# Kernel optimization log

Measured on AMD Instinct MI355X. Metric: run time of the kernel, lower is better.

The kernel has to match this reference:

```python
import jax, jax.numpy as jnp
import numpy as np

B, N, F_IN = 8, 4096, 128
H0, H1, OUT = 64, 32, 32
DENSITY = 0.004  # avg degree ~16


def setup_inputs() -> dict:
    key = jax.random.key(0)
    ks = jax.random.split(key, 8)
    x = jax.random.normal(ks[0], (B, N, F_IN), dtype=jnp.float32)
    # sparse binary adjacency (graph structure), stored dense as the module does
    adj = (jax.random.uniform(ks[1], (B, N, N)) < DENSITY).astype(jnp.float32)
    def w(k, i, o):
        return jax.random.normal(k, (i, o), dtype=jnp.float32) * (1.0 / np.sqrt(i))
    return {
        "x": x, "adj": adj,
        "Ws0": w(ks[2], F_IN, H0), "Wn0": w(ks[3], F_IN, H0), "b0": jnp.zeros((H0,), jnp.float32),
        "Ws1": w(ks[4], H0, H1),   "Wn1": w(ks[5], H0, H1),   "b1": jnp.zeros((H1,), jnp.float32),
        "Ws2": w(ks[6], H1, OUT),  "Wn2": w(ks[7], H1, OUT),  "b2": jnp.zeros((OUT,), jnp.float32),
    }


def _sage_layer(h, adj, deg_inv, Ws, Wn, b):
    # mean over incoming neighbors: row j of adj selects messages into node j
    neigh = jnp.einsum('bij,bjd->bid', adj, h) * deg_inv  # [B,N,d_in]
    return jax.nn.relu(h @ Ws + neigh @ Wn + b)


def reference(x, adj, Ws0, Wn0, b0, Ws1, Wn1, b1, Ws2, Wn2, b2):
    deg = jnp.sum(adj, axis=-1, keepdims=True)  # [B,N,1] in-degree
    deg_inv = 1.0 / jnp.maximum(deg, 1.0)
    h = _sage_layer(x, adj, deg_inv, Ws0, Wn0, b0)
    h = _sage_layer(h, adj, deg_inv, Ws1, Wn1, b1)
    h = _sage_layer(h, adj, deg_inv, Ws2, Wn2, b2)
    # original flattens to [B*N, out_dim] embeddings
    return h.reshape(B * N, -1)
```

## Files before the change

### kernel.cpp

```cpp
#include <hip/hip_runtime.h>
#include <hip/hip_bf16.h>

#define BN      32768
#define NCOL    4096
#define MAX_NBR 64

#define WS_NBR 0
#define WS_DEG (4*1024*1024)
#define WS_H0  (WS_DEG + 131072)
#define WS_H1  (WS_H0 + 8*1024*1024)

__global__ __launch_bounds__(256) void build_csr_kernel(
    const float* __restrict__ adj,
    unsigned short* __restrict__ nbr,
    int* __restrict__ deg)
{
    const int wave = threadIdx.x >> 6, lane = threadIdx.x & 63;
    const int row  = (blockIdx.x << 2) + wave;
    const float4* arow = reinterpret_cast<const float4*>(adj + (size_t)row * NCOL);
    unsigned short* outrow = nbr + (size_t)row * MAX_NBR;
    const unsigned long long below = (1ull << lane) - 1ull;

    int cnt = 0;
    #pragma unroll 4
    for (int t = 0; t < 16; ++t) {
        const int c = t * 64 + lane;
        const float4 q = arow[c];
        const float v[4] = { q.x, q.y, q.z, q.w };
        #pragma unroll
        for (int e = 0; e < 4; ++e) {
            const bool nz = (v[e] != 0.0f);
            const unsigned long long m = __ballot(nz);
            if (nz) {
                const int pos = cnt + (int)__popcll(m & below);
                if (pos < MAX_NBR) outrow[pos] = (unsigned short)(c * 4 + e);
            }
            cnt += (int)__popcll(m);
        }
    }
    if (lane == 0) deg[row] = cnt;
}

template<int D_IN, int D_OUT>
__global__ __launch_bounds__(256) void gather_layer_kernel(
    const float* __restrict__ hin,
    const unsigned short* __restrict__ nbr,
    const int* __restrict__ deg,
    const float* __restrict__ Ws, const float* __restrict__ Wn,
    const float* __restrict__ bias,
    float* __restrict__ hout)
{
    __shared__ float s_self[4][D_IN];
    __shared__ float s_neigh[4][D_IN];
    const int wave = threadIdx.x >> 6, lane = threadIdx.x & 63;
    const int row  = (blockIdx.x << 2) + wave;
    const int jbase = row & ~(NCOL - 1);

    const int d   = deg[row];
    const int cnt = d < MAX_NBR ? d : MAX_NBR;
    const float dinv = 1.0f / (float)(d > 1 ? d : 1);
    int mycol = 0;
    if (lane < cnt) mycol = nbr[(size_t)row * MAX_NBR + lane];

    if constexpr (D_IN == 128) {
        const float2 sf = *(const float2*)(hin + (size_t)row * D_IN + 2 * lane);
        float n0 = 0.f, n1 = 0.f;
        for (int t = 0; t < cnt; ++t) {
            const int j = jbase + __shfl(mycol, t, 64);
            const float2 f = *(const float2*)(hin + (size_t)j * D_IN + 2 * lane);
            n0 += f.x; n1 += f.y;
        }
        s_self[wave][2 * lane]     = sf.x;
        s_self[wave][2 * lane + 1] = sf.y;
        s_neigh[wave][2 * lane]     = n0 * dinv;
        s_neigh[wave][2 * lane + 1] = n1 * dinv;
    } else {
        float sv = 0.f, nv = 0.f;
        if (lane < D_IN) sv = hin[(size_t)row * D_IN + lane];
        for (int t = 0; t < cnt; ++t) {
            const int j = jbase + __shfl(mycol, t, 64);
            if (lane < D_IN) nv += hin[(size_t)j * D_IN + lane];
        }
        if (lane < D_IN) { s_self[wave][lane] = sv; s_neigh[wave][lane] = nv * dinv; }
    }
    __syncthreads();

    constexpr int SEG  = 64 / D_OUT;
    constexpr int KSEG = D_IN / SEG;
    const int o = lane % D_OUT, seg = lane / D_OUT;
    float acc = 0.f;
    #pragma unroll 8
    for (int kk = 0; kk < KSEG; ++kk) {
        const int k = seg * KSEG + kk;
        acc = fmaf(s_self[wave][k],  Ws[k * D_OUT + o], acc);
        acc = fmaf(s_neigh[wave][k], Wn[k * D_OUT + o], acc);
    }
    if constexpr (SEG == 2) acc += __shfl_xor(acc, 32, 64);
    if (seg == 0)
        hout[(size_t)row * D_OUT + o] = fmaxf(acc + bias[o], 0.f);
}

extern "C" void kernel_launch(void* const* d_in, const int* in_sizes, int n_in,
                              void* d_out, int out_size, void* d_ws, size_t ws_size,
                              hipStream_t stream) {
    const float* x   = (const float*)d_in[0];
    const float* adj = (const float*)d_in[1];
    const float* Ws0 = (const float*)d_in[2]; const float* Wn0 = (const float*)d_in[3];
    const float* b0  = (const float*)d_in[4];
    const float* Ws1 = (const float*)d_in[5]; const float* Wn1 = (const float*)d_in[6];
    const float* b1  = (const float*)d_in[7];
    const float* Ws2 = (const float*)d_in[8]; const float* Wn2 = (const float*)d_in[9];
    const float* b2  = (const float*)d_in[10];

    char* ws = (char*)d_ws;
    unsigned short* nbr = (unsigned short*)(ws + WS_NBR);
    int*   deg = (int*)(ws + WS_DEG);
    float* h0  = (float*)(ws + WS_H0);
    float* h1  = (float*)(ws + WS_H1);

    const int blocks = BN / 4;

    build_csr_kernel<<<blocks, 256, 0, stream>>>(adj, nbr, deg);
    gather_layer_kernel<128, 64><<<blocks, 256, 0, stream>>>(
        x,  nbr, deg, Ws0, Wn0, b0, h0);
    gather_layer_kernel<64, 32><<<blocks, 256, 0, stream>>>(
        h0, nbr, deg, Ws1, Wn1, b1, h1);
    gather_layer_kernel<32, 32><<<blocks, 256, 0, stream>>>(
        h1, nbr, deg, Ws2, Wn2, b2, (float*)d_out);
}
```

Baseline: 912.7 us.

## Split neighbor gather across all waves of a block, one row per block

Each gather-layer block now handles a single row, and its neighbor list is split across four waves (and sub-wave streams for narrow features). Partial sums are combined through shared memory before wave 0 does the small dense projection. This shortens the serial dependent-load chain per row. In exchange it launches four times as many blocks, adds an extra barrier, and leaves three waves idle during the matvec.

```diff
diff --git a/kernel.cpp b/kernel.cpp
--- a/kernel.cpp
+++ b/kernel.cpp
@@ -50,54 +50,80 @@
     const float* __restrict__ bias,
     float* __restrict__ hout)
 {
-    __shared__ float s_self[4][D_IN];
-    __shared__ float s_neigh[4][D_IN];
-    const int wave = threadIdx.x >> 6, lane = threadIdx.x & 63;
-    const int row  = (blockIdx.x << 2) + wave;
+    constexpr int SUB = (D_IN >= 64) ? 1 : (64 / D_IN);
+    constexpr int KPL = (D_IN + 63) / 64;
+    constexpr int NW  = 4 * SUB;
+    __shared__ float s_self[D_IN];
+    __shared__ float s_part[NW][D_IN];
+    __shared__ float s_neigh[D_IN];
+
+    const int tid  = threadIdx.x;
+    const int wave = tid >> 6, lane = tid & 63;
+    const int sub  = (D_IN < 64) ? (lane / D_IN) : 0;
+    const int sl   = (D_IN < 64) ? (lane % D_IN) : lane;
+    const int strm = wave * SUB + sub;
+    const int row  = blockIdx.x;
     const int jbase = row & ~(NCOL - 1);
 
     const int d   = deg[row];
     const int cnt = d < MAX_NBR ? d : MAX_NBR;
     const float dinv = 1.0f / (float)(d > 1 ? d : 1);
+
     int mycol = 0;
     if (lane < cnt) mycol = nbr[(size_t)row * MAX_NBR + lane];
 
-    if constexpr (D_IN == 128) {
-        const float2 sf = *(const float2*)(hin + (size_t)row * D_IN + 2 * lane);
-        float n0 = 0.f, n1 = 0.f;
-        for (int t = 0; t < cnt; ++t) {
-            const int j = jbase + __shfl(mycol, t, 64);
+    if (wave == 0) {
+        if constexpr (KPL == 2) {
+            const float2 f = *(const float2*)(hin + (size_t)row * D_IN + 2 * lane);
+            s_self[2 * lane] = f.x; s_self[2 * lane + 1] = f.y;
+        } else {
+            if (lane < D_IN) s_self[lane] = hin[(size_t)row * D_IN + lane];
+        }
+    }
+
+    float nv[KPL];
+    #pragma unroll
+    for (int i = 0; i < KPL; ++i) nv[i] = 0.f;
+    for (int t = strm; t < cnt; t += NW) {
+        const int j = jbase + __shfl(mycol, t, 64);
+        if constexpr (KPL == 2) {
             const float2 f = *(const float2*)(hin + (size_t)j * D_IN + 2 * lane);
-            n0 += f.x; n1 += f.y;
+            nv[0] += f.x; nv[1] += f.y;
+        } else {
+            nv[0] += hin[(size_t)j * D_IN + sl];
         }
-        s_self[wave][2 * lane]     = sf.x;
-        s_self[wave][2 * lane + 1] = sf.y;
-        s_neigh[wave][2 * lane]     = n0 * dinv;
-        s_neigh[wave][2 * lane + 1] = n1 * dinv;
+    }
+    if constexpr (KPL == 2) {
+        s_part[strm][2 * lane]     = nv[0];
+        s_part[strm][2 * lane + 1] = nv[1];
     } else {
-        float sv = 0.f, nv = 0.f;
-        if (lane < D_IN) sv = hin[(size_t)row * D_IN + lane];
-        for (int t = 0; t < cnt; ++t) {
-            const int j = jbase + __shfl(mycol, t, 64);
-            if (lane < D_IN) nv += hin[(size_t)j * D_IN + lane];
-        }
-        if (lane < D_IN) { s_self[wave][lane] = sv; s_neigh[wave][lane] = nv * dinv; }
+        s_part[strm][sl] = nv[0];
     }
     __syncthreads();
 
-    constexpr int SEG  = 64 / D_OUT;
-    constexpr int KSEG = D_IN / SEG;
-    const int o = lane % D_OUT, seg = lane / D_OUT;
-    float acc = 0.f;
-    #pragma unroll 8
-    for (int kk = 0; kk < KSEG; ++kk) {
-        const int k = seg * KSEG + kk;
-        acc = fmaf(s_self[wave][k],  Ws[k * D_OUT + o], acc);
-        acc = fmaf(s_neigh[wave][k], Wn[k * D_OUT + o], acc);
+    if (tid < D_IN) {
+        float s = 0.f;
+        #pragma unroll
+        for (int p = 0; p < NW; ++p) s += s_part[p][tid];
+        s_neigh[tid] = s * dinv;
     }
-    if constexpr (SEG == 2) acc += __shfl_xor(acc, 32, 64);
-    if (seg == 0)
-        hout[(size_t)row * D_OUT + o] = fmaxf(acc + bias[o], 0.f);
+    __syncthreads();
+
+    if (wave == 0) {
+        constexpr int SEG  = 64 / D_OUT;
+        constexpr int KSEG = D_IN / SEG;
+        const int o = lane % D_OUT, seg = lane / D_OUT;
+        float acc = 0.f;
+        #pragma unroll 8
+        for (int kk = 0; kk < KSEG; ++kk) {
+            const int k = seg * KSEG + kk;
+            acc = fmaf(s_self[k],  Ws[k * D_OUT + o], acc);
+            acc = fmaf(s_neigh[k], Wn[k * D_OUT + o], acc);
+        }
+        if constexpr (SEG == 2) acc += __shfl_xor(acc, 32, 64);
+        if (seg == 0)
+            hout[(size_t)row * D_OUT + o] = fmaxf(acc + bias[o], 0.f);
+    }
 }
 
 extern "C" void kernel_launch(void* const* d_in, const int* in_sizes, int n_in,
@@ -118,13 +144,11 @@
     float* h0  = (float*)(ws + WS_H0);
     float* h1  = (float*)(ws + WS_H1);
 
-    const int blocks = BN / 4;
-
-    build_csr_kernel<<<blocks, 256, 0, stream>>>(adj, nbr, deg);
-    gather_layer_kernel<128, 64><<<blocks, 256, 0, stream>>>(
+    build_csr_kernel<<<BN / 4, 256, 0, stream>>>(adj, nbr, deg);
+    gather_layer_kernel<128, 64><<<BN, 256, 0, stream>>>(
         x,  nbr, deg, Ws0, Wn0, b0, h0);
-    gather_layer_kernel<64, 32><<<blocks, 256, 0, stream>>>(
+    gather_layer_kernel<64, 32><<<BN, 256, 0, stream>>>(
         h0, nbr, deg, Ws1, Wn1, b1, h1);
-    gather_layer_kernel<32, 32><<<blocks, 256, 0, stream>>>(
+    gather_layer_kernel<32, 32><<<BN, 256, 0, stream>>>(
         h1, nbr, deg, Ws2, Wn2, b2, (float*)d_out);
 }
```

Measured after the change: 908.4 us. Within noise of the previous version (-0.5%).
